# Performance work log

Measured on AMD Instinct MI355X. Metric: run time of the kernel, lower is better.

## Reference

```python
import jax, jax.numpy as jnp
import numpy as np

BLOCK = 128
QMAX = 127.0


def _quant_dequant_act(x2d):
    """Dynamic per-token, per-128-column-group INT8 quantize + dequantize.

    x2d: [T, K]. Groups of shape 1x128 along K (is_weight=False path).
    """
    T, K = x2d.shape
    xb = x2d.reshape(T, K // BLOCK, BLOCK)
    amax = jnp.max(jnp.abs(xb), axis=-1, keepdims=True)
    scale = jnp.where(amax > 0, amax / QMAX, 1.0)
    q = jnp.clip(jnp.round(xb / scale), -QMAX, QMAX)  # int8 values
    return (q * scale).reshape(T, K)


def _quant_dequant_weight(w):
    """128x128 blockwise INT8 quantize + dequantize (is_weight=True path).

    w: [O, K] with O, K multiples of 128.
    """
    O, K = w.shape
    wb = w.reshape(O // BLOCK, BLOCK, K // BLOCK, BLOCK)
    amax = jnp.max(jnp.abs(wb), axis=(1, 3), keepdims=True)
    scale = jnp.where(amax > 0, amax / QMAX, 1.0)
    q = jnp.clip(jnp.round(wb / scale), -QMAX, QMAX)
    return (q * scale).reshape(O, K)


def setup_inputs() -> dict:
    key = jax.random.key(0)
    k1, k2, k3 = jax.random.split(key, 3)
    B, S, K, O = 4, 2048, 4096, 11008
    x = jax.random.normal(k1, (B, S, K), dtype=jnp.float32)
    w = jax.random.normal(k2, (O, K), dtype=jnp.float32) * 0.02
    bias = jax.random.normal(k3, (O,), dtype=jnp.float32) * 0.01
    return {"x": x, "w": w, "bias": bias}


def reference(x, w, bias):
    """INT8Linear forward: dynamic per-token INT8 activation quantization +
    128x128 blockwise-scaled INT8 weight GEMM + bias.

    Because scales are constant within each (token-group x weight-block),
    the blockwise-scaled int8 GEMM is mathematically identical to
    dequantize-then-matmul, which is the efficient dense expression here.
    """
    in_shape = x.shape
    x2d = x.reshape(-1, in_shape[-1])        # [T, K]
    xdq = _quant_dequant_act(x2d)            # [T, K]
    wdq = _quant_dequant_weight(w)           # [O, K]
    y = jnp.einsum('tk,ok->to', xdq, wdq) + bias
    return y.reshape(*in_shape[:-1], w.shape[0])
```

## Files before the change

kernel.cpp:

```cpp
#include <hip/hip_runtime.h>
#include <hip/hip_bf16.h>
#include <stdint.h>

#define QMAXF 127.0f

typedef __attribute__((ext_vector_type(4))) float f32x4;
typedef __attribute__((ext_vector_type(4))) int i32x4;

typedef __attribute__((address_space(1))) void gbl_void;
typedef __attribute__((address_space(3))) void lds_void;

__device__ __forceinline__ void gload_lds16(const void* g, void* l) {
    __builtin_amdgcn_global_load_lds((const gbl_void*)g, (lds_void*)l, 16, 0, 0);
}

__global__ __launch_bounds__(256) void qd_x_kernel(const float* __restrict__ x,
                                                   char* __restrict__ qx,
                                                   float* __restrict__ sxT,
                                                   long ngroups, int nkb, int T) {
    long gw = ((long)blockIdx.x * blockDim.x + threadIdx.x) >> 6;
    int lane = threadIdx.x & 63;
    if (gw >= ngroups) return;

    float2 v = *(reinterpret_cast<const float2*>(x) + gw * 64 + lane);
    float a = fmaxf(fabsf(v.x), fabsf(v.y));
#pragma unroll
    for (int off = 32; off; off >>= 1) a = fmaxf(a, __shfl_xor(a, off));

    float scale = a > 0.f ? a / QMAXF : 1.f;
    int q0 = (int)fminf(fmaxf(rintf(v.x / scale), -QMAXF), QMAXF);
    int q1 = (int)fminf(fmaxf(rintf(v.y / scale), -QMAXF), QMAXF);
    unsigned short packed = (unsigned short)((q0 & 0xFF) | ((q1 & 0xFF) << 8));
    reinterpret_cast<unsigned short*>(qx)[gw * 64 + lane] = packed;

    if (lane == 0) {
        int t = (int)(gw / nkb), kb = (int)(gw - (long)t * nkb);
        sxT[(size_t)kb * T + t] = scale;
    }
}

__global__ __launch_bounds__(256) void qd_w_kernel(const float* __restrict__ w,
                                                   char* __restrict__ qw,
                                                   float* __restrict__ sw,
                                                   int K, int nkb) {
    int kb = blockIdx.x, ob = blockIdx.y;
    size_t base = (size_t)ob * 128 * K + (size_t)kb * 128;
    int t = threadIdx.x;

    float4 v[16];
    float a = 0.f;
#pragma unroll
    for (int i = 0; i < 16; i++) {
        int f = i * 256 + t;
        int row = f >> 5, c4 = f & 31;
        v[i] = *reinterpret_cast<const float4*>(w + base + (size_t)row * K + c4 * 4);
        a = fmaxf(a, fmaxf(fmaxf(fabsf(v[i].x), fabsf(v[i].y)),
                           fmaxf(fabsf(v[i].z), fabsf(v[i].w))));
    }
#pragma unroll
    for (int off = 32; off; off >>= 1) a = fmaxf(a, __shfl_xor(a, off));

    __shared__ float red[4];
    if ((t & 63) == 0) red[t >> 6] = a;
    __syncthreads();
    a = fmaxf(fmaxf(red[0], red[1]), fmaxf(red[2], red[3]));

    float scale = a > 0.f ? a / QMAXF : 1.f;
    if (t == 0) sw[(size_t)ob * nkb + kb] = scale;
#pragma unroll
    for (int i = 0; i < 16; i++) {
        int f = i * 256 + t;
        int row = f >> 5, c4 = f & 31;
        int q0 = (int)fminf(fmaxf(rintf(v[i].x / scale), -QMAXF), QMAXF);
        int q1 = (int)fminf(fmaxf(rintf(v[i].y / scale), -QMAXF), QMAXF);
        int q2 = (int)fminf(fmaxf(rintf(v[i].z / scale), -QMAXF), QMAXF);
        int q3 = (int)fminf(fmaxf(rintf(v[i].w / scale), -QMAXF), QMAXF);
        unsigned int p = (q0 & 0xFF) | ((q1 & 0xFF) << 8) | ((q2 & 0xFF) << 16) |
                         ((unsigned int)(q3 & 0xFF) << 24);
        *reinterpret_cast<unsigned int*>(qw + base + (size_t)row * K + c4 * 4) = p;
    }
}

#define GBM 256
#define GBN 256
#define SUBK 64
#define A_BY 16384
#define B_BY 16384
#define SX_BY 1024
#define SLOT_BY (A_BY + B_BY + SX_BY)
#define RING 3

#define BAR()                              \
    do {                                   \
        asm volatile("" ::: "memory");     \
        __builtin_amdgcn_s_barrier();      \
        asm volatile("" ::: "memory");     \
    } while (0)
#define WAITL0()                                          \
    do {                                                  \
        asm volatile("s_waitcnt lgkmcnt(0)" ::: "memory");\
        __builtin_amdgcn_sched_barrier(0);                \
    } while (0)
#define WAITV(n) asm volatile("s_waitcnt vmcnt(" #n ")" ::: "memory")

__global__ __launch_bounds__(512, 1) void gemm_i8_kernel(
    const char* __restrict__ Aq,
    const char* __restrict__ Bq,
    const float* __restrict__ sxT,
    const float* __restrict__ swp,
    const float* __restrict__ bias,
    float* __restrict__ C,
    int M, int N, int K) {
    __shared__ alignas(16) unsigned char lds8[RING * SLOT_BY];

    int nTm = M / GBM, nTn = N / GBN;
    int nwg = gridDim.x, wg = blockIdx.x;
    int mt, nt;
    if ((nTm & 7) == 0 && (32 % (nTm >> 3)) == 0) {
        int x = wg & 7, j = wg >> 3;
        int mper = nTm >> 3;
        int G = 32 / mper;
        int wsz = mper * G;
        int fullw = nTn / G;
        int jfull = fullw * wsz;
        int g, r, width;
        if (j < jfull) { g = j / wsz; r = j - g * wsz; width = G; }
        else { g = fullw; r = j - jfull; width = nTn - fullw * G; }
        mt = x * mper + r / width;
        nt = g * G + r % width;
    } else {
        int swz = (nwg & 7) ? wg : ((wg & 7) * (nwg >> 3) + (wg >> 3));
        mt = swz / nTn; nt = swz - mt * nTn;
    }

    int t = threadIdx.x, wid = t >> 6, lane = t & 63;
    int wm = wid >> 2, wn = wid & 3;
    int lr = lane & 15, lq = lane >> 4;
    int nkb = K >> 7;
    int NSUB = K / SUBK;

    const char* Abase = Aq + (size_t)mt * GBM * K;
    const char* Bbase = Bq + (size_t)nt * GBN * K;

    {
    }
    int rA0 = t >> 2;
    int pcc = t & 3;
    int cA0 = (pcc ^ ((rA0 >> 1) & 3)) << 4;
    const char* gA = Abase + (size_t)rA0 * K + cA0;
    const char* gB = Bbase + (size_t)rA0 * K + cA0;
    const char* gSX = (const char*)sxT + ((size_t)mt * GBM + (t & 63) * 4) * 4;
    size_t rowStep = (size_t)128 * K;

    auto STAGE = [&](int slot, int j) {
        size_t kb = (size_t)j * SUBK;
        unsigned char* sb = lds8 + slot * SLOT_BY;
        gload_lds16(gA + kb, sb + t * 16);
        gload_lds16(gA + rowStep + kb, sb + (512 + t) * 16);
        gload_lds16(gB + kb, sb + A_BY + t * 16);
        gload_lds16(gB + rowStep + kb, sb + A_BY + (512 + t) * 16);
        gload_lds16(gSX + (size_t)(j >> 1) * M * 4, sb + A_BY + B_BY + (t & 63) * 16);
    };

    int physXor = (lq ^ ((lr >> 1) & 3)) << 4;
    int offA[2][4], offB[4], offSX[2][4];
#pragma unroll
    for (int mq = 0; mq < 2; mq++)
#pragma unroll
        for (int m = 0; m < 4; m++) {
            int row = wm * 128 + mq * 64 + m * 16;
            offA[mq][m] = (row + lr) * 64 + physXor;
            offSX[mq][m] = A_BY + B_BY + (row + lq * 4) * 4;
        }
#pragma unroll
    for (int n = 0; n < 4; n++)
        offB[n] = A_BY + (wn * 64 + n * 16 + lr) * 64 + physXor;

    f32x4 facc[8][4];
#pragma unroll
    for (int m = 0; m < 8; m++)
#pragma unroll
        for (int n = 0; n < 4; n++) facc[m][n] = (f32x4){0.f, 0.f, 0.f, 0.f};

    float swv = (lane < nkb) ? swp[(size_t)(nt * 2 + (wn >> 1)) * nkb + lane] : 0.f;

    auto COMPUTE = [&](int slot, float swq) {
        const unsigned char* sb = lds8 + slot * SLOT_BY;
        i32x4 b[4];
#pragma unroll
        for (int n = 0; n < 4; n++)
            b[n] = *reinterpret_cast<const i32x4*>(sb + offB[n]);
#pragma unroll
        for (int mq = 0; mq < 2; mq++) {
            i32x4 a[4];
            f32x4 sx4[4];
#pragma unroll
            for (int m = 0; m < 4; m++)
                a[m] = *reinterpret_cast<const i32x4*>(sb + offA[mq][m]);
#pragma unroll
            for (int m = 0; m < 4; m++)
                sx4[m] = *reinterpret_cast<const f32x4*>(sb + offSX[mq][m]);
            WAITL0();
            __builtin_amdgcn_s_setprio(1);
#pragma unroll
            for (int nq = 0; nq < 2; nq++) {
                i32x4 ia[4][2];
#pragma unroll
                for (int m = 0; m < 4; m++)
#pragma unroll
                    for (int n2 = 0; n2 < 2; n2++)
                        ia[m][n2] = __builtin_amdgcn_mfma_i32_16x16x64_i8(
                            a[m], b[nq * 2 + n2], (i32x4){0, 0, 0, 0}, 0, 0, 0);
#pragma unroll
                for (int m = 0; m < 4; m++) {
                    f32x4 s = sx4[m] * swq;
#pragma unroll
                    for (int n2 = 0; n2 < 2; n2++) {
                        f32x4 cv;
#pragma unroll
                        for (int r = 0; r < 4; r++) cv[r] = (float)ia[m][n2][r];
                        facc[mq * 4 + m][nq * 2 + n2] += cv * s;
                    }
                }
            }
            __builtin_amdgcn_s_setprio(0);
        }
    };

    STAGE(0, 0);
    STAGE(1, 1);

    for (int j = 0; j < NSUB; ++j) {
        WAITV(5);
        BAR();
        int jn = j + 2 > NSUB - 1 ? NSUB - 1 : j + 2;
        STAGE((j + 2) % RING, jn);
        float swq = __shfl(swv, j >> 1);
        COMPUTE(j % RING, swq);
    }
    asm volatile("s_waitcnt vmcnt(0)" ::: "memory");

    float bvv[4];
#pragma unroll
    for (int n = 0; n < 4; n++) bvv[n] = bias[nt * GBN + wn * 64 + n * 16 + lr];

#pragma unroll
    for (int m = 0; m < 8; m++) {
#pragma unroll
        for (int r = 0; r < 4; r++) {
            size_t row = (size_t)(mt * GBM + wm * 128 + m * 16 + lq * 4 + r);
            float* Crow = C + row * N + nt * GBN + wn * 64 + lr;
#pragma unroll
            for (int n = 0; n < 4; n++) Crow[n * 16] = facc[m][n][r] + bvv[n];
        }
    }
}

extern "C" void kernel_launch(void* const* d_in, const int* in_sizes, int n_in,
                              void* d_out, int out_size, void* d_ws, size_t ws_size,
                              hipStream_t stream) {
    const float* x = (const float*)d_in[0];
    const float* w = (const float*)d_in[1];
    const float* bias = (const float*)d_in[2];
    float* y = (float*)d_out;

    int O = in_sizes[2];
    int K = in_sizes[1] / O;
    int T = in_sizes[0] / K;
    int nkb = K / 128;

    char* qx = (char*)d_ws;
    size_t off = ((size_t)T * K + 255) & ~(size_t)255;
    char* qw = (char*)d_ws + off;
    off += ((size_t)O * K + 255) & ~(size_t)255;
    float* sxT = (float*)((char*)d_ws + off);
    off += ((size_t)nkb * T * 4 + 255) & ~(size_t)255;
    float* sw = (float*)((char*)d_ws + off);

    long ngroups = (long)T * nkb;
    qd_x_kernel<<<dim3((unsigned)((ngroups + 3) / 4)), dim3(256), 0, stream>>>(
        x, qx, sxT, ngroups, nkb, T);
    qd_w_kernel<<<dim3(nkb, O / 128), dim3(256), 0, stream>>>(w, qw, sw, K, nkb);

    int grid = (T / GBM) * (O / GBN);
    gemm_i8_kernel<<<dim3(grid), dim3(512), 0, stream>>>(qx, qw, sxT, sw, bias, y,
                                                         T, O, K);
}
```

Baseline: 809.4 us.

## Restructure int8 GEMM main loop to 128-wide K steps with double buffering

The GEMM now stages a full 128-column K block per iteration, a whole scale group, into a two-slot LDS ring instead of a three-slot ring of 64-column sub-steps. It uses a new XOR swizzle for 128-byte rows and chains two MFMAs per output tile before scaling. Interleaved LDS reads, the next-block global prefetch and partial lgkmcnt waits are placed by hand between MFMA groups. The intent is to halve the per-group int-to-float scaling work and the barrier count, and to overlap LDS reads with MFMA work, at the cost of shallower global prefetch and higher register pressure.

```diff
diff --git a/kernel.cpp b/kernel.cpp
--- a/kernel.cpp
+++ b/kernel.cpp
@@ -81,14 +81,10 @@
     }
 }
 
-#define GBM 256
-#define GBN 256
-#define SUBK 64
-#define A_BY 16384
-#define B_BY 16384
+#define A_BY 32768
+#define B_BY 32768
 #define SX_BY 1024
 #define SLOT_BY (A_BY + B_BY + SX_BY)
-#define RING 3
 
 #define BAR()                              \
     do {                                   \
@@ -96,12 +92,13 @@
         __builtin_amdgcn_s_barrier();      \
         asm volatile("" ::: "memory");     \
     } while (0)
-#define WAITL0()                                          \
-    do {                                                  \
-        asm volatile("s_waitcnt lgkmcnt(0)" ::: "memory");\
-        __builtin_amdgcn_sched_barrier(0);                \
+#define LGKM(n)                                               \
+    do {                                                      \
+        asm volatile("s_waitcnt lgkmcnt(" #n ")" ::: "memory");\
+        __builtin_amdgcn_sched_barrier(0);                    \
     } while (0)
-#define WAITV(n) asm volatile("s_waitcnt vmcnt(" #n ")" ::: "memory")
+#define WAITV0() asm volatile("s_waitcnt vmcnt(0)" ::: "memory")
+#define SCHED0() __builtin_amdgcn_sched_barrier(0)
 
 __global__ __launch_bounds__(512, 1) void gemm_i8_kernel(
     const char* __restrict__ Aq,
@@ -111,14 +108,14 @@
     const float* __restrict__ bias,
     float* __restrict__ C,
     int M, int N, int K) {
-    __shared__ alignas(16) unsigned char lds8[RING * SLOT_BY];
-
-    int nTm = M / GBM, nTn = N / GBN;
+    __shared__ alignas(16) unsigned char lds8[2 * SLOT_BY];
+
+    int nTm = M >> 8, nTn = N >> 8;
     int nwg = gridDim.x, wg = blockIdx.x;
     int mt, nt;
-    if ((nTm & 7) == 0 && (32 % (nTm >> 3)) == 0) {
+    int mper = nTm >> 3;
+    if ((nTm & 7) == 0 && mper > 0 && (32 % mper) == 0) {
         int x = wg & 7, j = wg >> 3;
-        int mper = nTm >> 3;
         int G = 32 / mper;
         int wsz = mper * G;
         int fullw = nTn / G;
@@ -137,44 +134,34 @@
     int wm = wid >> 2, wn = wid & 3;
     int lr = lane & 15, lq = lane >> 4;
     int nkb = K >> 7;
-    int NSUB = K / SUBK;
-
-    const char* Abase = Aq + (size_t)mt * GBM * K;
-    const char* Bbase = Bq + (size_t)nt * GBN * K;
-
-    {
-    }
-    int rA0 = t >> 2;
-    int pcc = t & 3;
-    int cA0 = (pcc ^ ((rA0 >> 1) & 3)) << 4;
-    const char* gA = Abase + (size_t)rA0 * K + cA0;
-    const char* gB = Bbase + (size_t)rA0 * K + cA0;
-    const char* gSX = (const char*)sxT + ((size_t)mt * GBM + (t & 63) * 4) * 4;
-    size_t rowStep = (size_t)128 * K;
-
-    auto STAGE = [&](int slot, int j) {
-        size_t kb = (size_t)j * SUBK;
+
+    const char* Abase = Aq + (size_t)mt * 256 * K;
+    const char* Bbase = Bq + (size_t)nt * 256 * K;
+
+    int rl0 = t >> 3;
+    int gc0 = ((t & 7) ^ (rl0 & 7)) * 16;
+
+    auto STAGE = [&](int slot, int i) {
+        size_t kb = (size_t)i << 7;
         unsigned char* sb = lds8 + slot * SLOT_BY;
-        gload_lds16(gA + kb, sb + t * 16);
-        gload_lds16(gA + rowStep + kb, sb + (512 + t) * 16);
-        gload_lds16(gB + kb, sb + A_BY + t * 16);
-        gload_lds16(gB + rowStep + kb, sb + A_BY + (512 + t) * 16);
-        gload_lds16(gSX + (size_t)(j >> 1) * M * 4, sb + A_BY + B_BY + (t & 63) * 16);
-    };
-
-    int physXor = (lq ^ ((lr >> 1) & 3)) << 4;
-    int offA[2][4], offB[4], offSX[2][4];
-#pragma unroll
-    for (int mq = 0; mq < 2; mq++)
-#pragma unroll
-        for (int m = 0; m < 4; m++) {
-            int row = wm * 128 + mq * 64 + m * 16;
-            offA[mq][m] = (row + lr) * 64 + physXor;
-            offSX[mq][m] = A_BY + B_BY + (row + lq * 4) * 4;
-        }
-#pragma unroll
-    for (int n = 0; n < 4; n++)
-        offB[n] = A_BY + (wn * 64 + n * 16 + lr) * 64 + physXor;
+        const char* ga = Abase + kb + (size_t)rl0 * K + gc0;
+        const char* gb = Bbase + kb + (size_t)rl0 * K + gc0;
+#pragma unroll
+        for (int h = 0; h < 4; h++) {
+            gload_lds16(ga + (size_t)(64 * h) * K, sb + (512 * h + t) * 16);
+            gload_lds16(gb + (size_t)(64 * h) * K, sb + A_BY + (512 * h + t) * 16);
+        }
+        if (wid == 0) {
+            const char* gs = (const char*)(sxT + (size_t)i * M + mt * 256 + lane * 4);
+            gload_lds16(gs, sb + A_BY + B_BY + lane * 16);
+        }
+    };
+
+    int xo0 = ((lq ^ (lr & 7)) << 4);
+    int xo1 = (((4 + lq) ^ (lr & 7)) << 4);
+    int rowA = wm * 128 + lr;
+    int rowB = wn * 64 + lr;
+    int sxoff = A_BY + B_BY + (wm * 128 + lq * 4) * 4;
 
     f32x4 facc[8][4];
 #pragma unroll
@@ -184,72 +171,103 @@
 
     float swv = (lane < nkb) ? swp[(size_t)(nt * 2 + (wn >> 1)) * nkb + lane] : 0.f;
 
-    auto COMPUTE = [&](int slot, float swq) {
-        const unsigned char* sb = lds8 + slot * SLOT_BY;
-        i32x4 b[4];
-#pragma unroll
-        for (int n = 0; n < 4; n++)
-            b[n] = *reinterpret_cast<const i32x4*>(sb + offB[n]);
-#pragma unroll
-        for (int mq = 0; mq < 2; mq++) {
-            i32x4 a[4];
-            f32x4 sx4[4];
-#pragma unroll
-            for (int m = 0; m < 4; m++)
-                a[m] = *reinterpret_cast<const i32x4*>(sb + offA[mq][m]);
-#pragma unroll
-            for (int m = 0; m < 4; m++)
-                sx4[m] = *reinterpret_cast<const f32x4*>(sb + offSX[mq][m]);
-            WAITL0();
-            __builtin_amdgcn_s_setprio(1);
-#pragma unroll
-            for (int nq = 0; nq < 2; nq++) {
-                i32x4 ia[4][2];
-#pragma unroll
-                for (int m = 0; m < 4; m++)
-#pragma unroll
-                    for (int n2 = 0; n2 < 2; n2++)
-                        ia[m][n2] = __builtin_amdgcn_mfma_i32_16x16x64_i8(
-                            a[m], b[nq * 2 + n2], (i32x4){0, 0, 0, 0}, 0, 0, 0);
-#pragma unroll
-                for (int m = 0; m < 4; m++) {
-                    f32x4 s = sx4[m] * swq;
-#pragma unroll
-                    for (int n2 = 0; n2 < 2; n2++) {
-                        f32x4 cv;
-#pragma unroll
-                        for (int r = 0; r < 4; r++) cv[r] = (float)ia[m][n2][r];
-                        facc[mq * 4 + m][nq * 2 + n2] += cv * s;
-                    }
-                }
+    i32x4 A0[4], A1[4], b0[4], b1[4];
+    f32x4 sxE[2], sxO[2];
+
+    auto RDA = [&](i32x4* dst, const unsigned char* sb, int mp) {
+#pragma unroll
+        for (int mm = 0; mm < 2; mm++) {
+            int rb = (rowA + (mp * 2 + mm) * 16) * 128;
+            dst[mm * 2 + 0] = *reinterpret_cast<const i32x4*>(sb + rb + xo0);
+            dst[mm * 2 + 1] = *reinterpret_cast<const i32x4*>(sb + rb + xo1);
+        }
+    };
+    auto RDB = [&](i32x4* dst, const unsigned char* sb, int nq) {
+#pragma unroll
+        for (int nn = 0; nn < 2; nn++) {
+            int rb = A_BY + (rowB + (nq * 2 + nn) * 16) * 128;
+            dst[nn * 2 + 0] = *reinterpret_cast<const i32x4*>(sb + rb + xo0);
+            dst[nn * 2 + 1] = *reinterpret_cast<const i32x4*>(sb + rb + xo1);
+        }
+    };
+    auto RDSX = [&](f32x4* s, const unsigned char* sb, int mp) {
+#pragma unroll
+        for (int mm = 0; mm < 2; mm++)
+            s[mm] = *reinterpret_cast<const f32x4*>(sb + sxoff + (mp * 2 + mm) * 64);
+    };
+    auto MF = [&](i32x4* Aa, i32x4* Bb, int mp, int nq, f32x4* s, float swq) {
+        __builtin_amdgcn_s_setprio(1);
+#pragma unroll
+        for (int mm = 0; mm < 2; mm++) {
+            f32x4 sc = s[mm] * swq;
+#pragma unroll
+            for (int nn = 0; nn < 2; nn++) {
+                i32x4 ia = __builtin_amdgcn_mfma_i32_16x16x64_i8(
+                    Aa[mm * 2 + 0], Bb[nn * 2 + 0], (i32x4){0, 0, 0, 0}, 0, 0, 0);
+                ia = __builtin_amdgcn_mfma_i32_16x16x64_i8(
+                    Aa[mm * 2 + 1], Bb[nn * 2 + 1], ia, 0, 0, 0);
+                f32x4& f = facc[mp * 2 + mm][nq * 2 + nn];
+#pragma unroll
+                for (int r = 0; r < 4; r++) f[r] += (float)ia[r] * sc[r];
             }
-            __builtin_amdgcn_s_setprio(0);
-        }
+        }
+        __builtin_amdgcn_s_setprio(0);
     };
 
     STAGE(0, 0);
-    STAGE(1, 1);
-
-    for (int j = 0; j < NSUB; ++j) {
-        WAITV(5);
+    WAITV0();
+    BAR();
+
+    for (int i = 0; i < nkb; ++i) {
+        const unsigned char* sb = lds8 + (i & 1) * SLOT_BY;
+        float swq = __shfl(swv, i);
+
+        RDSX(sxE, sb, 0);
+        RDA(A0, sb, 0);
+        RDB(b0, sb, 0);
+        RDB(b1, sb, 1);
+        SCHED0();
+        RDA(A1, sb, 1);
+        LGKM(4);
+        MF(A0, b0, 0, 0, sxE, swq);
+        SCHED0();
+        RDSX(sxO, sb, 1);
+        if (i + 1 < nkb) STAGE((i + 1) & 1, i + 1);
+        SCHED0();
+        MF(A0, b1, 0, 1, sxE, swq);
+        SCHED0();
+        RDA(A0, sb, 2);
+        LGKM(4);
+        MF(A1, b1, 1, 1, sxO, swq);
+        SCHED0();
+        RDSX(sxE, sb, 2);
+        SCHED0();
+        MF(A1, b0, 1, 0, sxO, swq);
+        SCHED0();
+        RDA(A1, sb, 3);
+        LGKM(4);
+        MF(A0, b0, 2, 0, sxE, swq);
+        SCHED0();
+        RDSX(sxO, sb, 3);
+        SCHED0();
+        MF(A0, b1, 2, 1, sxE, swq);
+        LGKM(0);
+        MF(A1, b1, 3, 1, sxO, swq);
+        MF(A1, b0, 3, 0, sxO, swq);
+        WAITV0();
         BAR();
-        int jn = j + 2 > NSUB - 1 ? NSUB - 1 : j + 2;
-        STAGE((j + 2) % RING, jn);
-        float swq = __shfl(swv, j >> 1);
-        COMPUTE(j % RING, swq);
-    }
-    asm volatile("s_waitcnt vmcnt(0)" ::: "memory");
+    }
 
     float bvv[4];
 #pragma unroll
-    for (int n = 0; n < 4; n++) bvv[n] = bias[nt * GBN + wn * 64 + n * 16 + lr];
+    for (int n = 0; n < 4; n++) bvv[n] = bias[nt * 256 + wn * 64 + n * 16 + lr];
 
 #pragma unroll
     for (int m = 0; m < 8; m++) {
 #pragma unroll
         for (int r = 0; r < 4; r++) {
-            size_t row = (size_t)(mt * GBM + wm * 128 + m * 16 + lq * 4 + r);
-            float* Crow = C + row * N + nt * GBN + wn * 64 + lr;
+            size_t row = (size_t)(mt * 256 + wm * 128 + m * 16 + lq * 4 + r);
+            float* Crow = C + row * N + nt * 256 + wn * 64 + lr;
 #pragma unroll
             for (int n = 0; n < 4; n++) Crow[n * 16] = facc[m][n][r] + bvv[n];
         }
@@ -282,7 +300,7 @@
         x, qx, sxT, ngroups, nkb, T);
     qd_w_kernel<<<dim3(nkb, O / 128), dim3(256), 0, stream>>>(w, qw, sw, K, nkb);
 
-    int grid = (T / GBM) * (O / GBN);
+    int grid = (T / 256) * (O / 256);
     gemm_i8_kernel<<<dim3(grid), dim3(512), 0, stream>>>(qx, qw, sxT, sw, bias, y,
                                                          T, O, K);
 }
```

Result: slower. 1.052 ms (+30.0%).
